# Performance work log

Hardware: AMD Instinct MI355X
Metric: run time of the kernel (lower is better)

## Reference

```python
import jax, jax.numpy as jnp
import numpy as np

# ---- constants hard-coded in the torch module ----
NEG_EPS = 1e-30          # eps used in log clamps
TAU = 0.35               # near-field temperature (getattr default)
K0 = 128                 # near-field band width
C_EMBD, N_HEADS, RANK = 768, 12, 32
B, T = 1, 2048


def _lin(k, fin, fout):
    lim = 1.0 / np.sqrt(fin)
    return jax.random.uniform(k, (fin, fout), jnp.float32, -lim, lim)


def _bias(k, fin, fout):
    lim = 1.0 / np.sqrt(fin)
    return jax.random.uniform(k, (fout,), jnp.float32, -lim, lim)


def setup_inputs() -> dict:
    key = jax.random.key(0)
    ks = jax.random.split(key, 24)
    C, H, R = C_EMBD, N_HEADS, RANK
    return {
        "x": jax.random.normal(ks[0], (B, T, C), jnp.float32),
        "Wq_w": _lin(ks[1], C, C), "Wq_b": _bias(ks[2], C, C),
        "Wk_w": _lin(ks[3], C, C), "Wk_b": _bias(ks[4], C, C),
        "Wv_w": _lin(ks[5], C, C), "Wv_b": _bias(ks[6], C, C),
        "Wo_w": _lin(ks[7], C, C), "Wo_b": _bias(ks[8], C, C),
        "Pq_w": _lin(ks[9], C, R),
        "Pk_w": _lin(ks[10], C, R),
        "Pv_w": _lin(ks[11], C, R),
        "up_w": _lin(ks[12], R, C),
        "gate_u": jax.random.normal(ks[13], (H, C // H), jnp.float32),
        "gate_b": jnp.zeros((H,), jnp.float32),
        "Wz_w": _lin(ks[14], 4 * C, C), "Wz_b": _bias(ks[15], 4 * C, C),
    }


def reference(x, Wq_w, Wq_b, Wk_w, Wk_b, Wv_w, Wv_b, Wo_w, Wo_b,
              Pq_w, Pk_w, Pv_w, up_w, gate_u, gate_b, Wz_w, Wz_b):
    Bx, Tx, C = x.shape
    H = gate_u.shape[0]
    D = C // H
    R = Pq_w.shape[1]
    k0 = min(K0, Tx - 1)
    kernel = k0 + 1
    b_scalar = -np.log(max(Tx, 1)).astype(np.float32) if hasattr(np.log(1.0), 'astype') else -np.log(max(Tx, 1))
    b_scalar = jnp.float32(-np.log(max(Tx, 1)))

    # 0) projections + heads
    Q = x @ Wq_w + Wq_b
    K = x @ Wk_w + Wk_b
    V = x @ Wv_w + Wv_b
    heads = lambda z: z.reshape(Bx, Tx, H, D).transpose(0, 2, 1, 3)  # (B,H,T,D)
    Qh, Kh, Vh = heads(Q), heads(K), heads(V)

    idx = jnp.arange(Tx)
    causal = idx[None, :] <= idx[:, None]                  # (T,T)
    band = causal & ((idx[:, None] - idx[None, :]) <= k0)  # banded causal

    # 1) low-rank EA + sigmoid + LASER seed
    Qr, Kr, Vr = Q @ Pq_w, K @ Pk_w, V @ Pv_w              # (B,T,R)
    S = (Qr @ Kr.transpose(0, 2, 1)) * (1.0 / np.sqrt(R))  # (B,T,T)
    # masked logits were -1e9 -> sigmoid == 0 exactly in fp32
    A_seed = jnp.where(causal[None], jax.nn.sigmoid(S * S + b_scalar), 0.0)
    # running causal max over keys, per feature (== amax of causally masked keys)
    m_seed = jax.lax.cummax(Vr, axis=1)                    # (B,T,R)
    Yr = jnp.einsum('bij,bjr->bir', A_seed, jnp.exp(Vr)) * jnp.exp(-m_seed)
    H0 = (jnp.log(jnp.maximum(Yr, NEG_EPS)) + m_seed) @ up_w  # (B,T,C)

    # 2a) near-field banded causal attention (cos^2 / tau, sigmoid, LASER)
    l2n = lambda z: z / jnp.maximum(jnp.linalg.norm(z, axis=-1, keepdims=True), 1e-12)
    cos = jnp.einsum('bhid,bhjd->bhij', l2n(Qh), l2n(Kh))  # (B,H,T,T)
    A_near = jnp.where(band[None, None], jax.nn.sigmoid(cos * cos / TAU + b_scalar), 0.0)
    # sliding-window (width kernel, past-only) max of V per feature
    m_near = jax.lax.reduce_window(
        Vh, -jnp.inf, jax.lax.max,
        window_dimensions=(1, 1, kernel, 1), window_strides=(1, 1, 1, 1),
        padding=[(0, 0), (0, 0), (kernel - 1, 0), (0, 0)])   # (B,H,T,D)
    V_exp = jnp.exp(Vh - m_near)
    Y_near = jnp.einsum('bhij,bhjd->bhid', A_near, V_exp)
    H_near = jnp.log(jnp.maximum(Y_near, NEG_EPS)) + m_near

    # 2b) far-field hierarchical levels: source truncates mid-loop; the
    # accumulator H_far_total_h is initialized to zeros -> contributes zero.
    Ht_h = H_near                                          # (B,H,T,D)

    # 3) head-wise sigmoid gating
    g = jax.nn.sigmoid(jnp.einsum('bhtd,hd->bht', Ht_h, gate_u) + gate_b[None, :, None])
    Ht_h = Ht_h * g[..., None]
    Htilde = Ht_h.transpose(0, 2, 1, 3).reshape(Bx, Tx, C)

    # 4) GRU blend (Wz consumes 4*C features)
    z = jax.nn.sigmoid(jnp.concatenate([x, H0, Htilde, H0 * Htilde], axis=-1) @ Wz_w + Wz_b)
    H_out = (1.0 - z) * H0 + z * Htilde
    return H_out @ Wo_w + Wo_b
```

## Files before the change

kernel.cpp:

```cpp
#include <hip/hip_runtime.h>
#include <math.h>

static constexpr float B_SCALAR    = -7.6246189861593985f;
static constexpr float INV_TAU     = 2.8571428571428571f;
static constexpr float INV_SQRT_R  = 0.17677669529663687f;

typedef __attribute__((ext_vector_type(8))) short bf16x8;
typedef __attribute__((ext_vector_type(4))) float f32x4;

__device__ __forceinline__ unsigned short f2b(float f) {
    union { float f; unsigned int u; } v; v.f = f;
    unsigned int r = v.u + 0x7fffu + ((v.u >> 16) & 1u);
    return (unsigned short)(r >> 16);
}

typedef const __attribute__((address_space(1))) unsigned int* gp1_t;
typedef __attribute__((address_space(3))) unsigned int* lp3_t;
__device__ __forceinline__ void gload16(const unsigned short* g, unsigned short* l) {
    __builtin_amdgcn_global_load_lds((gp1_t)g, (lp3_t)l, 16, 0, 0);
}

__device__ __forceinline__ bf16x8 frag128(const unsigned short* base, int row, int elem) {
    int byte = (row * 128 + elem * 2) ^ ((row & 7) << 4);
    return *(const bf16x8*)((const char*)base + byte);
}
__device__ __forceinline__ bf16x8 frag384(const unsigned short* base, int row, int elem) {
    int byte = (row * 384 + elem * 2) ^ ((row & 7) << 4);
    return *(const bf16x8*)((const char*)base + byte);
}

template<int MODE, int KZ>
__global__ __launch_bounds__(256) void gemm_mfma(
    const unsigned short* __restrict__ A0, const unsigned short* __restrict__ A1,
    const unsigned short* __restrict__ A2, const unsigned short* __restrict__ A3,
    const unsigned short* __restrict__ Bt, const float* __restrict__ bias,
    float* __restrict__ outf, unsigned short* __restrict__ outb,
    float* __restrict__ pbuf, int K, int ldo)
{
    __shared__ unsigned short As[2][128*64];
    __shared__ unsigned short Bs[2][128*64];
    const int tid = threadIdx.x;
    const int lane = tid & 63, wid = tid >> 6;
    const int wr = wid >> 1, wc = wid & 1;
    const int fr = lane & 15, fq = lane >> 4;
    const int n0 = blockIdx.x * 128, m0 = blockIdx.y * 128;
    const int kz = blockIdx.z;
    const int kslice = K / KZ;
    const int kbase = kz * kslice;
    const int nt = kslice / 64;

    f32x4 acc[4][4];
#pragma unroll
    for (int mi = 0; mi < 4; ++mi)
#pragma unroll
        for (int ni = 0; ni < 4; ++ni) acc[mi][ni] = (f32x4){0.f, 0.f, 0.f, 0.f};

    auto stage = [&](int buf, int k0) {
        const unsigned short* Ap;
        int k0l, ldA;
        if (MODE == 1) {
            int p = k0 / 768;
            Ap = (p == 0) ? A0 : (p == 1) ? A1 : (p == 2) ? A2 : A3;
            k0l = k0 - p * 768; ldA = 768;
        } else { Ap = A0; k0l = k0; ldA = K; }
#pragma unroll
        for (int i = 0; i < 4; ++i) {
            int cb = i * 256 + wid * 64;
            int c  = cb + lane;
            int r = c >> 3;
            int col = ((c & 7) ^ (r & 7)) * 8;
            gload16(Ap + (size_t)(m0 + r) * ldA + k0l + col, &As[buf][cb * 8]);
            gload16(Bt + (size_t)(n0 + r) * K   + k0  + col, &Bs[buf][cb * 8]);
        }
    };

    stage(0, kbase);
    asm volatile("s_waitcnt vmcnt(0)" ::: "memory");
    __builtin_amdgcn_s_barrier();
    __builtin_amdgcn_sched_barrier(0);

    int cur = 0;
    for (int t = 0; t < nt; ++t) {
        if (t + 1 < nt) stage(cur ^ 1, kbase + (t + 1) * 64);
#pragma unroll
        for (int kk = 0; kk < 64; kk += 32) {
            bf16x8 af[4], bfr[4];
#pragma unroll
            for (int mi = 0; mi < 4; ++mi)
                af[mi] = frag128(As[cur], wr*64 + mi*16 + fr, kk + fq*8);
#pragma unroll
            for (int ni = 0; ni < 4; ++ni)
                bfr[ni] = frag128(Bs[cur], wc*64 + ni*16 + fr, kk + fq*8);
#pragma unroll
            for (int mi = 0; mi < 4; ++mi)
#pragma unroll
                for (int ni = 0; ni < 4; ++ni)
                    acc[mi][ni] = __builtin_amdgcn_mfma_f32_16x16x32_bf16(
                        af[mi], bfr[ni], acc[mi][ni], 0, 0, 0);
        }
        asm volatile("s_waitcnt vmcnt(0)" ::: "memory");
        __builtin_amdgcn_s_barrier();
        __builtin_amdgcn_sched_barrier(0);
        cur ^= 1;
    }
#pragma unroll
    for (int mi = 0; mi < 4; ++mi)
#pragma unroll
        for (int ni = 0; ni < 4; ++ni)
#pragma unroll
            for (int v = 0; v < 4; ++v) {
                int m = m0 + wr*64 + mi*16 + fq*4 + v;
                int n = n0 + wc*64 + ni*16 + fr;
                float val = acc[mi][ni][v];
                if (KZ > 1) {
                    pbuf[((size_t)kz * 2048 + m) * 768 + n] = val;
                } else {
                    float vv = val + bias[n];
                    outf[(size_t)m * ldo + n] = vv;
                    if (MODE == 0) outb[(size_t)m * ldo + n] = f2b(vv);
                }
            }
}

__global__ __launch_bounds__(256) void wz_combine(
    const float* __restrict__ pbuf, const float* __restrict__ bz,
    const float* __restrict__ h0, const float* __restrict__ htl,
    unsigned short* __restrict__ outb)
{
    int i = blockIdx.x * 256 + threadIdx.x;
    if (i >= 2048*768/4) return;
    float4 s = *(const float4*)&pbuf[i*4];
    float4 p1 = *(const float4*)&pbuf[1536*1024 + i*4];
    float4 p2 = *(const float4*)&pbuf[2*1536*1024 + i*4];
    float4 p3 = *(const float4*)&pbuf[3*1536*1024 + i*4];
    s.x += p1.x + p2.x + p3.x; s.y += p1.y + p2.y + p3.y;
    s.z += p1.z + p2.z + p3.z; s.w += p1.w + p2.w + p3.w;
    float4 b = *(const float4*)&bz[(i % 192) * 4];
    float4 a = *(const float4*)&h0[i*4];
    float4 t = *(const float4*)&htl[i*4];
    float z0 = 1.f/(1.f+expf(-(s.x+b.x))), z1 = 1.f/(1.f+expf(-(s.y+b.y)));
    float z2 = 1.f/(1.f+expf(-(s.z+b.z))), z3 = 1.f/(1.f+expf(-(s.w+b.w)));
    outb[i*4+0] = f2b((1.f-z0)*a.x + z0*t.x);
    outb[i*4+1] = f2b((1.f-z1)*a.y + z1*t.y);
    outb[i*4+2] = f2b((1.f-z2)*a.z + z2*t.z);
    outb[i*4+3] = f2b((1.f-z3)*a.w + z3*t.w);
}

__global__ __launch_bounds__(256) void wo_combine(
    const float* __restrict__ pbuf, const float* __restrict__ bo,
    float* __restrict__ out)
{
    int i = blockIdx.x * 256 + threadIdx.x;
    if (i >= 2048*768/4) return;
    float4 s = *(const float4*)&pbuf[i*4];
    float4 p1 = *(const float4*)&pbuf[1536*1024 + i*4];
    float4 b = *(const float4*)&bo[(i % 192) * 4];
    float4 o;
    o.x = s.x + p1.x + b.x; o.y = s.y + p1.y + b.y;
    o.z = s.z + p1.z + b.z; o.w = s.w + p1.w + b.w;
    *(float4*)&out[i*4] = o;
}

__global__ __launch_bounds__(256) void prep_all(
    const float* __restrict__ x, unsigned short* __restrict__ xb,
    const float* __restrict__ wq, const float* __restrict__ wk,
    const float* __restrict__ wv, unsigned short* __restrict__ wqkvT,
    const float* __restrict__ wz, unsigned short* __restrict__ wzT,
    const float* __restrict__ wo, unsigned short* __restrict__ woT,
    const float* __restrict__ pq, const float* __restrict__ pk,
    const float* __restrict__ pv, unsigned short* __restrict__ pT,
    const float* __restrict__ bq, const float* __restrict__ bk,
    const float* __restrict__ bv, float* __restrict__ bqkv)
{
    __shared__ float tile[32][33];
    int b = blockIdx.x;
    if (b < 1536) {
        int i = b * 256 + threadIdx.x;
        float4 v = *(const float4*)&x[i * 4];
        xb[i*4+0] = f2b(v.x); xb[i*4+1] = f2b(v.y);
        xb[i*4+2] = f2b(v.z); xb[i*4+3] = f2b(v.w);
        return;
    }
    b -= 1536;
    const float* src; unsigned short* dst; int K, N, tb;
    if (b < 1728) {
        int sel = b / 576;
        src = (sel == 0) ? wq : (sel == 1) ? wk : wv;
        dst = wqkvT + (size_t)sel * 768 * 768;
        K = 768; N = 768; tb = b - sel * 576;
    } else if (b < 4032) {
        src = wz; dst = wzT; K = 3072; N = 768; tb = b - 1728;
    } else if (b < 4608) {
        src = wo; dst = woT; K = 768; N = 768; tb = b - 4032;
    } else if (b < 4680) {
        int sel = (b - 4608) / 24;
        src = (sel == 0) ? pq : (sel == 1) ? pk : pv;
        dst = pT + (size_t)sel * 32 * 768;
        K = 768; N = 32; tb = (b - 4608) % 24;
    } else {
        int n = (b - 4680) * 256 + threadIdx.x;
        if (n < 2304)
            bqkv[n] = (n < 768) ? bq[n] : (n < 1536) ? bk[n - 768] : bv[n - 1536];
        return;
    }
    int kt = K / 32;
    int kb = (tb % kt) * 32, nb = (tb / kt) * 32;
    int tx = threadIdx.x & 31, ty = threadIdx.x >> 5;
#pragma unroll
    for (int s = 0; s < 32; s += 8)
        tile[ty + s][tx] = src[(size_t)(kb + ty + s) * N + nb + tx];
    __syncthreads();
#pragma unroll
    for (int s = 0; s < 32; s += 8)
        dst[(size_t)(nb + ty + s) * K + kb + tx] = f2b(tile[tx][ty + s]);
}

__global__ __launch_bounds__(256) void lowrank_mfma(
    const unsigned short* __restrict__ qkvb, const unsigned short* __restrict__ pT,
    float* __restrict__ pbuf)
{
    __shared__ unsigned short As[2][128*64];
    __shared__ unsigned short Bs[2][32*64];
    const int tid = threadIdx.x, lane = tid & 63, wid = tid >> 6;
    const int fr = lane & 15, fq = lane >> 4;
    const int m0 = blockIdx.x * 128;
    const int sel = blockIdx.y, kz = blockIdx.z;
    const int kbase = kz * 192;

    f32x4 acc[2][2];
#pragma unroll
    for (int mi = 0; mi < 2; ++mi)
#pragma unroll
        for (int ni = 0; ni < 2; ++ni) acc[mi][ni] = (f32x4){0.f,0.f,0.f,0.f};

    auto stage = [&](int buf, int k0) {
#pragma unroll
        for (int i = 0; i < 4; ++i) {
            int cb = i * 256 + wid * 64, c = cb + lane;
            int r = c >> 3, col = ((c & 7) ^ (r & 7)) * 8;
            gload16(qkvb + (size_t)(m0 + r) * 2304 + sel*768 + k0 + col, &As[buf][cb * 8]);
        }
        {
            int cb = wid * 64, c = cb + lane;
            int r = c >> 3, col = ((c & 7) ^ (r & 7)) * 8;
            gload16(pT + (size_t)sel * 32*768 + (size_t)r * 768 + k0 + col, &Bs[buf][cb * 8]);
        }
    };

    stage(0, kbase);
    asm volatile("s_waitcnt vmcnt(0)" ::: "memory");
    __builtin_amdgcn_s_barrier();
    __builtin_amdgcn_sched_barrier(0);

    int cur = 0;
    for (int t = 0; t < 3; ++t) {
        if (t + 1 < 3) stage(cur ^ 1, kbase + (t + 1) * 64);
#pragma unroll
        for (int kk = 0; kk < 64; kk += 32) {
            bf16x8 a[2], b[2];
#pragma unroll
            for (int mi = 0; mi < 2; ++mi)
                a[mi] = frag128(As[cur], wid*32 + mi*16 + fr, kk + fq*8);
#pragma unroll
            for (int ni = 0; ni < 2; ++ni)
                b[ni] = frag128(Bs[cur], ni*16 + fr, kk + fq*8);
#pragma unroll
            for (int mi = 0; mi < 2; ++mi)
#pragma unroll
                for (int ni = 0; ni < 2; ++ni)
                    acc[mi][ni] = __builtin_amdgcn_mfma_f32_16x16x32_bf16(
                        a[mi], b[ni], acc[mi][ni], 0, 0, 0);
        }
        asm volatile("s_waitcnt vmcnt(0)" ::: "memory");
        __builtin_amdgcn_s_barrier();
        __builtin_amdgcn_sched_barrier(0);
        cur ^= 1;
    }
#pragma unroll
    for (int mi = 0; mi < 2; ++mi)
#pragma unroll
        for (int ni = 0; ni < 2; ++ni)
#pragma unroll
            for (int v = 0; v < 4; ++v) {
                int m = m0 + wid*32 + mi*16 + fq*4 + v;
                int n = ni*16 + fr;
                pbuf[((size_t)(kz*3 + sel) * 2048 + m) * 32 + n] = acc[mi][ni][v];
            }
}

__global__ __launch_bounds__(256) void lowrank_finish(
    const float* __restrict__ pbuf,
    unsigned short* __restrict__ qrb, unsigned short* __restrict__ krb,
    float* __restrict__ vr, unsigned short* __restrict__ evtb)
{
    int idx = blockIdx.x * 256 + threadIdx.x;
    int sel = idx >> 16, rem = idx & 65535;
    float s = pbuf[(size_t)(0*3 + sel)*65536 + rem]
            + pbuf[(size_t)(1*3 + sel)*65536 + rem]
            + pbuf[(size_t)(2*3 + sel)*65536 + rem]
            + pbuf[(size_t)(3*3 + sel)*65536 + rem];
    if (sel == 0)      qrb[rem] = f2b(s * INV_SQRT_R);
    else if (sel == 1) krb[rem] = f2b(s);
    else {
        int t = rem >> 5, r = rem & 31;
        vr[rem] = s;
        evtb[(size_t)r * 2048 + t] = f2b(expf(s));
    }
}

__global__ __launch_bounds__(256) void cummax_vr(const float* __restrict__ vr,
                                                 float* __restrict__ ms)
{
    __shared__ float part[256];
    int r = blockIdx.x, tid = threadIdx.x;
    int t0 = tid * 8;
    float v[8];
    float run = -INFINITY;
#pragma unroll
    for (int e = 0; e < 8; ++e) { run = fmaxf(run, vr[(t0+e)*32 + r]); v[e] = run; }
    part[tid] = run;
    __syncthreads();
    for (int off = 1; off < 256; off <<= 1) {
        float other = (tid >= off) ? part[tid - off] : -INFINITY;
        __syncthreads();
        part[tid] = fmaxf(part[tid], other);
        __syncthreads();
    }
    float excl = (tid > 0) ? part[tid - 1] : -INFINITY;
#pragma unroll
    for (int e = 0; e < 8; ++e) ms[(t0+e)*32 + r] = fmaxf(v[e], excl);
}

__global__ __launch_bounds__(256) void seed_mfma(
    const unsigned short* __restrict__ qrb, const unsigned short* __restrict__ krb,
    const unsigned short* __restrict__ evtb, float* __restrict__ partial)
{
    int it = blockIdx.x, jc = blockIdx.y;
    if (jc > it) return;
    const int i0 = it * 128, j0 = jc * 128;
    __shared__ unsigned short Qs[128*32];
    __shared__ unsigned short Ks[128*32];
    __shared__ unsigned short Es[32*128];
    __shared__ unsigned short Ps[128*128];
    const int tid = threadIdx.x, lane = tid & 63, wid = tid >> 6;
    const int fr = lane & 15, fq = lane >> 4;

#pragma unroll
    for (int s = 0; s < 2; ++s) {
        int cb = s * 256 + wid * 64;
        int c = cb + lane;
        int r = c >> 2, col = (c & 3) * 8;
        gload16(qrb + (size_t)(i0 + r) * 32 + col, &Qs[cb * 8]);
        gload16(krb + (size_t)(j0 + r) * 32 + col, &Ks[cb * 8]);
    }
#pragma unroll
    for (int s = 0; s < 2; ++s) {
        int c = s * 256 + tid;
        int rr = c >> 4, cc = c & 15;
        bf16x8 v = *(const bf16x8*)&evtb[(size_t)rr * 2048 + j0 + cc * 8];
        int byte = (rr * 256 + cc * 16) ^ ((rr & 7) << 4);
        *(bf16x8*)((char*)Es + byte) = v;
    }
    __syncthreads();

    const int wr = wid >> 1, wc = wid & 1;
    bf16x8 af[4], bk[4];
#pragma unroll
    for (int mi = 0; mi < 4; ++mi)
        af[mi] = *(const bf16x8*)&Qs[(wr*64 + mi*16 + fr)*32 + fq*8];
#pragma unroll
    for (int ni = 0; ni < 4; ++ni)
        bk[ni] = *(const bf16x8*)&Ks[(wc*64 + ni*16 + fr)*32 + fq*8];
#pragma unroll
    for (int mi = 0; mi < 4; ++mi)
#pragma unroll
        for (int ni = 0; ni < 4; ++ni) {
            f32x4 s4 = __builtin_amdgcn_mfma_f32_16x16x32_bf16(
                af[mi], bk[ni], (f32x4){0.f,0.f,0.f,0.f}, 0, 0, 0);
#pragma unroll
            for (int v = 0; v < 4; ++v) {
                int row = wr*64 + mi*16 + fq*4 + v;
                int col = wc*64 + ni*16 + fr;
                float a = 0.f;
                if (j0 + col <= i0 + row) {
                    float s = s4[v];
                    a = 1.f / (1.f + expf(-(s*s + B_SCALAR)));
                }
                int byte = (row * 256 + col * 2) ^ ((row & 7) << 4);
                *(unsigned short*)((char*)Ps + byte) = f2b(a);
            }
        }
    __syncthreads();

    f32x4 yacc[2][2];
#pragma unroll
    for (int mi = 0; mi < 2; ++mi)
#pragma unroll
        for (int nf = 0; nf < 2; ++nf) yacc[mi][nf] = (f32x4){0.f,0.f,0.f,0.f};
#pragma unroll
    for (int ks = 0; ks < 4; ++ks) {
        bf16x8 pa[2], eb[2];
#pragma unroll
        for (int mi = 0; mi < 2; ++mi) {
            int row = wid*32 + mi*16 + fr;
            int byte = (row * 256 + ks * 64 + fq * 16) ^ ((row & 7) << 4);
            pa[mi] = *(const bf16x8*)((const char*)Ps + byte);
        }
#pragma unroll
        for (int nf = 0; nf < 2; ++nf) {
            int rrow = nf*16 + fr;
            int byte = (rrow * 256 + ks * 64 + fq * 16) ^ ((rrow & 7) << 4);
            eb[nf] = *(const bf16x8*)((const char*)Es + byte);
        }
#pragma unroll
        for (int mi = 0; mi < 2; ++mi)
#pragma unroll
            for (int nf = 0; nf < 2; ++nf)
                yacc[mi][nf] = __builtin_amdgcn_mfma_f32_16x16x32_bf16(
                    pa[mi], eb[nf], yacc[mi][nf], 0, 0, 0);
    }
    float* pout = partial + ((size_t)(it*16 + jc) * 128) * 32;
#pragma unroll
    for (int mi = 0; mi < 2; ++mi)
#pragma unroll
        for (int nf = 0; nf < 2; ++nf)
#pragma unroll
            for (int v = 0; v < 4; ++v) {
                int row = wid*32 + mi*16 + fq*4 + v;
                int col = nf*16 + fr;
                pout[row*32 + col] = yacc[mi][nf][v];
            }
}

__global__ __launch_bounds__(256) void seed_up(
    const float* __restrict__ partial, const float* __restrict__ ms,
    const float* __restrict__ up, float* __restrict__ h0,
    unsigned short* __restrict__ h0b)
{
    __shared__ float ls[32];
    int t = blockIdx.x, tid = threadIdx.x;
    if (tid < 32) {
        int r = tid;
        int it = t >> 7, row = t & 127;
        float y = 0.f;
        for (int jjc = 0; jjc <= it; ++jjc)
            y += partial[(((size_t)(it*16 + jjc) * 128) + row) * 32 + r];
        float m = ms[t*32 + r];
        ls[r] = logf(fmaxf(y * expf(-m), 1e-30f)) + m;
    }
    __syncthreads();
    for (int c = tid; c < 768; c += 256) {
        float acc = 0.f;
#pragma unroll
        for (int rr = 0; rr < 32; ++rr) acc = fmaf(ls[rr], up[rr*768 + c], acc);
        h0[(size_t)t*768 + c] = acc;
        h0b[(size_t)t*768 + c] = f2b(acc);
    }
}

__global__ void head_norms_write(const float* __restrict__ qkv,
                                 unsigned short* __restrict__ qhatb,
                                 unsigned short* __restrict__ khatb)
{
    int t = blockIdx.x, tid = threadIdx.x;
    int h = tid >> 6, d = tid & 63;
    float q = qkv[t*2304 + h*64 + d];
    float k = qkv[t*2304 + 768 + h*64 + d];
    float sq = q*q, sk = k*k;
#pragma unroll
    for (int off = 32; off; off >>= 1) { sq += __shfl_xor(sq, off); sk += __shfl_xor(sk, off); }
    float iq = 1.f / fmaxf(sqrtf(sq), 1e-12f);
    float ik = 1.f / fmaxf(sqrtf(sk), 1e-12f);
    qhatb[(size_t)t*768 + h*64 + d] = f2b(q * iq);
    khatb[(size_t)t*768 + h*64 + d] = f2b(k * ik);
}

__global__ __launch_bounds__(256) void slide_max(const float* __restrict__ qkv,
                                                 float* __restrict__ mnear,
                                                 unsigned short* __restrict__ vexptb)
{
    __shared__ float vs[192][64];
    int c0 = blockIdx.x * 64, t0 = blockIdx.y * 64;
    int tid = threadIdx.x;
#pragma unroll
    for (int s = 0; s < 12; ++s) {
        int idx = tid + s * 256;
        int rr = idx >> 4, c4 = (idx & 15) * 4;
        int t = t0 - 128 + rr;
        float4 v4;
        if (t < 0) v4 = make_float4(-INFINITY, -INFINITY, -INFINITY, -INFINITY);
        else       v4 = *(const float4*)&qkv[t*2304 + 1536 + c0 + c4];
        *(float4*)&vs[rr][c4] = v4;
    }
    __syncthreads();
    int c = tid & 63, tg = tid >> 6;
    const int TG = tg * 16;
    float core = -INFINITY;
    for (int s = TG + 15; s <= TG + 128; ++s) core = fmaxf(core, vs[s][c]);
    float head[16], tail[16];
    head[15] = -INFINITY;
    float hs = -INFINITY;
#pragma unroll
    for (int u = 14; u >= 0; --u) { hs = fmaxf(hs, vs[TG + u][c]); head[u] = hs; }
    tail[0] = -INFINITY;
    float ts = -INFINITY;
#pragma unroll
    for (int u = 1; u <= 15; ++u) { ts = fmaxf(ts, vs[TG + 128 + u][c]); tail[u] = ts; }
#pragma unroll
    for (int u = 0; u < 16; ++u) {
        int tl = TG + u;
        float m = fmaxf(fmaxf(core, head[u]), tail[u]);
        float v = vs[tl + 128][c];
        int t = t0 + tl;
        mnear[(size_t)t*768 + c0 + c] = m;
        vexptb[(size_t)(c0 + c) * 2048 + t] = f2b(expf(v - m));
    }
}

__global__ __launch_bounds__(256) void near_fused(
    const unsigned short* __restrict__ qhatb, const unsigned short* __restrict__ khatb,
    const unsigned short* __restrict__ vexptb, const float* __restrict__ mnear,
    const float* __restrict__ gu, const float* __restrict__ gb,
    const float* __restrict__ h0, float* __restrict__ hn,
    unsigned short* __restrict__ htlb, unsigned short* __restrict__ prodb)
{
    __shared__ unsigned short Qs[64*64];
    __shared__ unsigned short KPs[192*64];
    __shared__ unsigned short Vst[64*192];
    const int it = blockIdx.x, hh = blockIdx.y;
    const int i0 = it * 64;
    const int tid = threadIdx.x, lane = tid & 63, wid = tid >> 6;
    const int fr = lane & 15, fq = lane >> 4;

#pragma unroll
    for (int i = 0; i < 2; ++i) {
        int cb = i * 256 + wid * 64, c = cb + lane;
        int r = c >> 3, col = ((c & 7) ^ (r & 7)) * 8;
        gload16(qhatb + (size_t)(i0 + r) * 768 + hh*64 + col, &Qs[cb * 8]);
    }
#pragma unroll
    for (int i = 0; i < 6; ++i) {
        int cb = i * 256 + wid * 64, c = cb + lane;
        int r = c >> 3, col = ((c & 7) ^ (r & 7)) * 8;
        int j = i0 - 128 + r; if (j < 0) j = 0;
        gload16(khatb + (size_t)j * 768 + hh*64 + col, &KPs[cb * 8]);
    }
#pragma unroll
    for (int i = 0; i < 6; ++i) {
        int cb = i * 256 + wid * 64, c = cb + lane;
        int d = c / 24, cc = c - d * 24;
        int ccp = (cc & 24) | ((cc & 7) ^ (d & 7));
        int t = i0 - 128 + ccp * 8; if (t < 0) t = 0;
        gload16(vexptb + (size_t)(hh*64 + d) * 2048 + t, &Vst[cb * 8]);
    }
    __syncthreads();

    f32x4 sacc[4][3];
#pragma unroll
    for (int mi = 0; mi < 4; ++mi)
#pragma unroll
        for (int ni = 0; ni < 3; ++ni) sacc[mi][ni] = (f32x4){0.f,0.f,0.f,0.f};
#pragma unroll
    for (int kt = 0; kt < 2; ++kt) {
        int kk = kt * 32;
        bf16x8 qa[4], kb[3];
#pragma unroll
        for (int mi = 0; mi < 4; ++mi)
            qa[mi] = frag128(Qs, mi*16 + fr, kk + fq*8);
#pragma unroll
        for (int ni = 0; ni < 3; ++ni)
            kb[ni] = frag128(KPs, wid*48 + ni*16 + fr, kk + fq*8);
#pragma unroll
        for (int mi = 0; mi < 4; ++mi)
#pragma unroll
            for (int ni = 0; ni < 3; ++ni)
                sacc[mi][ni] = __builtin_amdgcn_mfma_f32_16x16x32_bf16(
                    qa[mi], kb[ni], sacc[mi][ni], 0, 0, 0);
    }
    __syncthreads();

#pragma unroll
    for (int mi = 0; mi < 4; ++mi)
#pragma unroll
        for (int ni = 0; ni < 3; ++ni)
#pragma unroll
            for (int v = 0; v < 4; ++v) {
                int il = mi*16 + fq*4 + v;
                int jl = wid*48 + ni*16 + fr;
                float s = sacc[mi][ni][v];
                float a = 0.f;
                if (jl >= il && jl <= il + 128 && (i0 - 128 + jl) >= 0)
                    a = 1.f / (1.f + expf(-(s*s*INV_TAU + B_SCALAR)));
                int byte = (il * 384 + jl * 2) ^ ((il & 7) << 4);
                *(unsigned short*)((char*)KPs + byte) = f2b(a);
            }
    __syncthreads();

    f32x4 yacc[4];
#pragma unroll
    for (int nf = 0; nf < 4; ++nf) yacc[nf] = (f32x4){0.f,0.f,0.f,0.f};
#pragma unroll
    for (int ks = 0; ks < 6; ++ks) {
        int kk = ks * 32;
        bf16x8 pa = frag384(KPs, wid*16 + fr, kk + fq*8);
        bf16x8 vb[4];
#pragma unroll
        for (int nf = 0; nf < 4; ++nf)
            vb[nf] = frag384(Vst, nf*16 + fr, kk + fq*8);
#pragma unroll
        for (int nf = 0; nf < 4; ++nf)
            yacc[nf] = __builtin_amdgcn_mfma_f32_16x16x32_bf16(pa, vb[nf], yacc[nf], 0, 0, 0);
    }

    float hv[4][4];
    float sp[4] = {0.f, 0.f, 0.f, 0.f};
#pragma unroll
    for (int nf = 0; nf < 4; ++nf) {
        int d = nf*16 + fr;
        float guv = gu[hh*64 + d];
#pragma unroll
        for (int v = 0; v < 4; ++v) {
            int row = wid*16 + fq*4 + v;
            float y = yacc[nf][v];
            float h = logf(fmaxf(y, 1e-30f)) + mnear[(size_t)(i0 + row)*768 + hh*64 + d];
            hv[nf][v] = h;
            sp[v] = fmaf(h, guv, sp[v]);
        }
    }
#pragma unroll
    for (int off = 1; off < 16; off <<= 1) {
#pragma unroll
        for (int v = 0; v < 4; ++v) sp[v] += __shfl_xor(sp[v], off);
    }
    float gbh = gb[hh];
#pragma unroll
    for (int v = 0; v < 4; ++v) sp[v] = 1.f / (1.f + expf(-(sp[v] + gbh)));
#pragma unroll
    for (int nf = 0; nf < 4; ++nf)
#pragma unroll
        for (int v = 0; v < 4; ++v) {
            int row = wid*16 + fq*4 + v;
            int d = nf*16 + fr;
            size_t idx = (size_t)(i0 + row)*768 + hh*64 + d;
            float htl = hv[nf][v] * sp[v];
            hn[idx] = htl;
            htlb[idx] = f2b(htl);
            prodb[idx] = f2b(h0[idx] * htl);
        }
}

extern "C" void kernel_launch(void* const* d_in, const int* in_sizes, int n_in,
                              void* d_out, int out_size, void* d_ws, size_t ws_size,
                              hipStream_t stream)
{
    const float* x  = (const float*)d_in[0];
    const float* wq = (const float*)d_in[1];  const float* bq = (const float*)d_in[2];
    const float* wk = (const float*)d_in[3];  const float* bk = (const float*)d_in[4];
    const float* wv = (const float*)d_in[5];  const float* bv = (const float*)d_in[6];
    const float* wo = (const float*)d_in[7];  const float* bo = (const float*)d_in[8];
    const float* pq = (const float*)d_in[9];  const float* pk = (const float*)d_in[10];
    const float* pv = (const float*)d_in[11];
    const float* up = (const float*)d_in[12];
    const float* gu = (const float*)d_in[13]; const float* gb = (const float*)d_in[14];
    const float* wz = (const float*)d_in[15]; const float* bz = (const float*)d_in[16];
    float* out = (float*)d_out;

    float* w = (float*)d_ws;
    float* qkv  = w; w += 2048*2304;
    float* vr   = w; w += 2048*32;
    float* ms   = w; w += 2048*32;
    float* h0   = w; w += 2048*768;
    float* mnear= w; w += 2048*768;
    float* hn   = w; w += 2048*768;
    float* partial = w; w += 16*16*128*32;
    float* pgemm = w; w += 4*2048*768;
    float* plr   = w; w += 4*3*2048*32;
    float* bqkv = w; w += 2304;
    unsigned short* xb     = (unsigned short*)w; w += 2048*768/2;
    unsigned short* qkvb   = (unsigned short*)w; w += 2048*2304/2;
    unsigned short* wqkvT  = (unsigned short*)w; w += 2304*768/2;
    unsigned short* wzT    = (unsigned short*)w; w += 768*3072/2;
    unsigned short* woT    = (unsigned short*)w; w += 768*768/2;
    unsigned short* pT     = (unsigned short*)w; w += 3*32*768/2;
    unsigned short* h0b    = (unsigned short*)w; w += 2048*768/2;
    unsigned short* htlb   = (unsigned short*)w; w += 2048*768/2;
    unsigned short* prodb  = (unsigned short*)w; w += 2048*768/2;
    unsigned short* houtb  = (unsigned short*)w; w += 2048*768/2;
    unsigned short* qrb    = (unsigned short*)w; w += 2048*32/2;
    unsigned short* krb    = (unsigned short*)w; w += 2048*32/2;
    unsigned short* evtb   = (unsigned short*)w; w += 32*2048/2;
    unsigned short* qhatb  = (unsigned short*)w; w += 2048*768/2;
    unsigned short* khatb  = (unsigned short*)w; w += 2048*768/2;
    unsigned short* vexptb = (unsigned short*)w; w += 768*2048/2;

    prep_all<<<6225, 256, 0, stream>>>(x, xb, wq, wk, wv, wqkvT, wz, wzT,
                                       wo, woT, pq, pk, pv, pT, bq, bk, bv, bqkv);

    gemm_mfma<0,1><<<dim3(18,16,1), 256, 0, stream>>>(xb, nullptr, nullptr, nullptr,
        wqkvT, bqkv, qkv, qkvb, nullptr, 768, 2304);

    lowrank_mfma<<<dim3(16,3,4), 256, 0, stream>>>(qkvb, pT, plr);
    lowrank_finish<<<768, 256, 0, stream>>>(plr, qrb, krb, vr, evtb);
    cummax_vr<<<32, 256, 0, stream>>>(vr, ms);
    seed_mfma<<<dim3(16,16), 256, 0, stream>>>(qrb, krb, evtb, partial);
    seed_up<<<2048, 256, 0, stream>>>(partial, ms, up, h0, h0b);

    head_norms_write<<<2048, 768, 0, stream>>>(qkv, qhatb, khatb);
    slide_max<<<dim3(12,32), 256, 0, stream>>>(qkv, mnear, vexptb);
    near_fused<<<dim3(32,12), 256, 0, stream>>>(qhatb, khatb, vexptb, mnear,
                                                gu, gb, h0, hn, htlb, prodb);

    gemm_mfma<1,4><<<dim3(6,16,4), 256, 0, stream>>>(xb, h0b, htlb, prodb,
        wzT, nullptr, nullptr, nullptr, pgemm, 3072, 768);
    wz_combine<<<1536, 256, 0, stream>>>(pgemm, bz, h0, hn, houtb);
    gemm_mfma<2,2><<<dim3(6,16,2), 256, 0, stream>>>(houtb, nullptr, nullptr, nullptr,
        woT, nullptr, nullptr, nullptr, pgemm, 768, 768);
    wo_combine<<<1536, 256, 0, stream>>>(pgemm, bo, out);
}
```

Baseline: 148.2 us.

## Halve GEMM M-tile and merge small post-processing kernels into fewer launches

The shared GEMM kernel drops from 128x128 to 64x128 output tiles, doubling grid rows so more workgroups fill the device's compute units for these modest-sized matmuls. In exchange each block reuses its B tile over fewer rows. lowrank_finish and cummax_vr are merged into one kernel that reduces the Vr partials and runs the cumulative max directly, which removes the vr buffer and one launch. head_norms_write and slide_max are also fused into a single launch that picks its role from the block index.

```diff
diff --git a/kernel.cpp b/kernel.cpp
--- a/kernel.cpp
+++ b/kernel.cpp
@@ -37,21 +37,21 @@
     float* __restrict__ outf, unsigned short* __restrict__ outb,
     float* __restrict__ pbuf, int K, int ldo)
 {
-    __shared__ unsigned short As[2][128*64];
+    __shared__ unsigned short As[2][64*64];
     __shared__ unsigned short Bs[2][128*64];
     const int tid = threadIdx.x;
     const int lane = tid & 63, wid = tid >> 6;
     const int wr = wid >> 1, wc = wid & 1;
     const int fr = lane & 15, fq = lane >> 4;
-    const int n0 = blockIdx.x * 128, m0 = blockIdx.y * 128;
+    const int n0 = blockIdx.x * 128, m0 = blockIdx.y * 64;
     const int kz = blockIdx.z;
     const int kslice = K / KZ;
     const int kbase = kz * kslice;
     const int nt = kslice / 64;
 
-    f32x4 acc[4][4];
-#pragma unroll
-    for (int mi = 0; mi < 4; ++mi)
+    f32x4 acc[2][4];
+#pragma unroll
+    for (int mi = 0; mi < 2; ++mi)
 #pragma unroll
         for (int ni = 0; ni < 4; ++ni) acc[mi][ni] = (f32x4){0.f, 0.f, 0.f, 0.f};
 
@@ -64,13 +64,18 @@
             k0l = k0 - p * 768; ldA = 768;
         } else { Ap = A0; k0l = k0; ldA = K; }
 #pragma unroll
-        for (int i = 0; i < 4; ++i) {
-            int cb = i * 256 + wid * 64;
-            int c  = cb + lane;
+        for (int i = 0; i < 2; ++i) {
+            int cb = i * 256 + wid * 64, c = cb + lane;
             int r = c >> 3;
             int col = ((c & 7) ^ (r & 7)) * 8;
             gload16(Ap + (size_t)(m0 + r) * ldA + k0l + col, &As[buf][cb * 8]);
-            gload16(Bt + (size_t)(n0 + r) * K   + k0  + col, &Bs[buf][cb * 8]);
+        }
+#pragma unroll
+        for (int i = 0; i < 4; ++i) {
+            int cb = i * 256 + wid * 64, c = cb + lane;
+            int r = c >> 3;
+            int col = ((c & 7) ^ (r & 7)) * 8;
+            gload16(Bt + (size_t)(n0 + r) * K + k0 + col, &Bs[buf][cb * 8]);
         }
     };
 
@@ -84,15 +89,15 @@
         if (t + 1 < nt) stage(cur ^ 1, kbase + (t + 1) * 64);
 #pragma unroll
         for (int kk = 0; kk < 64; kk += 32) {
-            bf16x8 af[4], bfr[4];
-#pragma unroll
-            for (int mi = 0; mi < 4; ++mi)
-                af[mi] = frag128(As[cur], wr*64 + mi*16 + fr, kk + fq*8);
+            bf16x8 af[2], bfr[4];
+#pragma unroll
+            for (int mi = 0; mi < 2; ++mi)
+                af[mi] = frag128(As[cur], wr*32 + mi*16 + fr, kk + fq*8);
 #pragma unroll
             for (int ni = 0; ni < 4; ++ni)
                 bfr[ni] = frag128(Bs[cur], wc*64 + ni*16 + fr, kk + fq*8);
 #pragma unroll
-            for (int mi = 0; mi < 4; ++mi)
+            for (int mi = 0; mi < 2; ++mi)
 #pragma unroll
                 for (int ni = 0; ni < 4; ++ni)
                     acc[mi][ni] = __builtin_amdgcn_mfma_f32_16x16x32_bf16(
@@ -104,12 +109,12 @@
         cur ^= 1;
     }
 #pragma unroll
-    for (int mi = 0; mi < 4; ++mi)
+    for (int mi = 0; mi < 2; ++mi)
 #pragma unroll
         for (int ni = 0; ni < 4; ++ni)
 #pragma unroll
             for (int v = 0; v < 4; ++v) {
-                int m = m0 + wr*64 + mi*16 + fq*4 + v;
+                int m = m0 + wr*32 + mi*16 + fq*4 + v;
                 int n = n0 + wc*64 + ni*16 + fr;
                 float val = acc[mi][ni][v];
                 if (KZ > 1) {
@@ -288,36 +293,39 @@
             }
 }
 
-__global__ __launch_bounds__(256) void lowrank_finish(
+__global__ __launch_bounds__(256) void lowrank_post(
     const float* __restrict__ pbuf,
     unsigned short* __restrict__ qrb, unsigned short* __restrict__ krb,
-    float* __restrict__ vr, unsigned short* __restrict__ evtb)
-{
-    int idx = blockIdx.x * 256 + threadIdx.x;
-    int sel = idx >> 16, rem = idx & 65535;
-    float s = pbuf[(size_t)(0*3 + sel)*65536 + rem]
-            + pbuf[(size_t)(1*3 + sel)*65536 + rem]
-            + pbuf[(size_t)(2*3 + sel)*65536 + rem]
-            + pbuf[(size_t)(3*3 + sel)*65536 + rem];
-    if (sel == 0)      qrb[rem] = f2b(s * INV_SQRT_R);
-    else if (sel == 1) krb[rem] = f2b(s);
-    else {
-        int t = rem >> 5, r = rem & 31;
-        vr[rem] = s;
-        evtb[(size_t)r * 2048 + t] = f2b(expf(s));
-    }
-}
-
-__global__ __launch_bounds__(256) void cummax_vr(const float* __restrict__ vr,
-                                                 float* __restrict__ ms)
-{
+    unsigned short* __restrict__ evtb, float* __restrict__ ms)
+{
+    int b = blockIdx.x, tid = threadIdx.x;
+    if (b < 512) {
+        int idx = b * 256 + tid;
+        int sel = idx >> 16, rem = idx & 65535;
+        float s = pbuf[(size_t)(0*3 + sel)*65536 + rem]
+                + pbuf[(size_t)(1*3 + sel)*65536 + rem]
+                + pbuf[(size_t)(2*3 + sel)*65536 + rem]
+                + pbuf[(size_t)(3*3 + sel)*65536 + rem];
+        if (sel == 0) qrb[rem] = f2b(s * INV_SQRT_R);
+        else          krb[rem] = f2b(s);
+        return;
+    }
     __shared__ float part[256];
-    int r = blockIdx.x, tid = threadIdx.x;
+    int r = b - 512;
     int t0 = tid * 8;
-    float v[8];
+    float sv[8], v[8];
     float run = -INFINITY;
 #pragma unroll
-    for (int e = 0; e < 8; ++e) { run = fmaxf(run, vr[(t0+e)*32 + r]); v[e] = run; }
+    for (int e = 0; e < 8; ++e) {
+        int t = t0 + e;
+        float s = pbuf[(size_t)(0*3 + 2)*65536 + t*32 + r]
+                + pbuf[(size_t)(1*3 + 2)*65536 + t*32 + r]
+                + pbuf[(size_t)(2*3 + 2)*65536 + t*32 + r]
+                + pbuf[(size_t)(3*3 + 2)*65536 + t*32 + r];
+        sv[e] = s;
+        run = fmaxf(run, s);
+        v[e] = run;
+    }
     part[tid] = run;
     __syncthreads();
     for (int off = 1; off < 256; off <<= 1) {
@@ -328,7 +336,11 @@
     }
     float excl = (tid > 0) ? part[tid - 1] : -INFINITY;
 #pragma unroll
-    for (int e = 0; e < 8; ++e) ms[(t0+e)*32 + r] = fmaxf(v[e], excl);
+    for (int e = 0; e < 8; ++e) {
+        int t = t0 + e;
+        ms[t*32 + r] = fmaxf(v[e], excl);
+        evtb[(size_t)r * 2048 + t] = f2b(expf(sv[e]));
+    }
 }
 
 __global__ __launch_bounds__(256) void seed_mfma(
@@ -458,30 +470,30 @@
     }
 }
 
-__global__ void head_norms_write(const float* __restrict__ qkv,
-                                 unsigned short* __restrict__ qhatb,
-                                 unsigned short* __restrict__ khatb)
-{
-    int t = blockIdx.x, tid = threadIdx.x;
-    int h = tid >> 6, d = tid & 63;
-    float q = qkv[t*2304 + h*64 + d];
-    float k = qkv[t*2304 + 768 + h*64 + d];
-    float sq = q*q, sk = k*k;
-#pragma unroll
-    for (int off = 32; off; off >>= 1) { sq += __shfl_xor(sq, off); sk += __shfl_xor(sk, off); }
-    float iq = 1.f / fmaxf(sqrtf(sq), 1e-12f);
-    float ik = 1.f / fmaxf(sqrtf(sk), 1e-12f);
-    qhatb[(size_t)t*768 + h*64 + d] = f2b(q * iq);
-    khatb[(size_t)t*768 + h*64 + d] = f2b(k * ik);
-}
-
-__global__ __launch_bounds__(256) void slide_max(const float* __restrict__ qkv,
-                                                 float* __restrict__ mnear,
-                                                 unsigned short* __restrict__ vexptb)
+__global__ __launch_bounds__(256) void norms_slide(
+    const float* __restrict__ qkv,
+    unsigned short* __restrict__ qhatb, unsigned short* __restrict__ khatb,
+    float* __restrict__ mnear, unsigned short* __restrict__ vexptb)
 {
     __shared__ float vs[192][64];
-    int c0 = blockIdx.x * 64, t0 = blockIdx.y * 64;
-    int tid = threadIdx.x;
+    int b = blockIdx.x, tid = threadIdx.x;
+    if (b < 6144) {
+        int w = b * 4 + (tid >> 6);
+        int lane = tid & 63;
+        int t = w / 12, h = w - t * 12;
+        float q = qkv[t*2304 + h*64 + lane];
+        float k = qkv[t*2304 + 768 + h*64 + lane];
+        float sq = q*q, sk = k*k;
+#pragma unroll
+        for (int off = 32; off; off >>= 1) { sq += __shfl_xor(sq, off); sk += __shfl_xor(sk, off); }
+        float iq = 1.f / fmaxf(sqrtf(sq), 1e-12f);
+        float ik = 1.f / fmaxf(sqrtf(sk), 1e-12f);
+        qhatb[(size_t)t*768 + h*64 + lane] = f2b(q * iq);
+        khatb[(size_t)t*768 + h*64 + lane] = f2b(k * ik);
+        return;
+    }
+    b -= 6144;
+    int c0 = (b % 12) * 64, t0 = (b / 12) * 64;
 #pragma unroll
     for (int s = 0; s < 12; ++s) {
         int idx = tid + s * 256;
@@ -667,7 +679,6 @@
 
     float* w = (float*)d_ws;
     float* qkv  = w; w += 2048*2304;
-    float* vr   = w; w += 2048*32;
     float* ms   = w; w += 2048*32;
     float* h0   = w; w += 2048*768;
     float* mnear= w; w += 2048*768;
@@ -696,24 +707,22 @@
     prep_all<<<6225, 256, 0, stream>>>(x, xb, wq, wk, wv, wqkvT, wz, wzT,
                                        wo, woT, pq, pk, pv, pT, bq, bk, bv, bqkv);
 
-    gemm_mfma<0,1><<<dim3(18,16,1), 256, 0, stream>>>(xb, nullptr, nullptr, nullptr,
+    gemm_mfma<0,1><<<dim3(18,32,1), 256, 0, stream>>>(xb, nullptr, nullptr, nullptr,
         wqkvT, bqkv, qkv, qkvb, nullptr, 768, 2304);
 
     lowrank_mfma<<<dim3(16,3,4), 256, 0, stream>>>(qkvb, pT, plr);
-    lowrank_finish<<<768, 256, 0, stream>>>(plr, qrb, krb, vr, evtb);
-    cummax_vr<<<32, 256, 0, stream>>>(vr, ms);
+    lowrank_post<<<544, 256, 0, stream>>>(plr, qrb, krb, evtb, ms);
     seed_mfma<<<dim3(16,16), 256, 0, stream>>>(qrb, krb, evtb, partial);
     seed_up<<<2048, 256, 0, stream>>>(partial, ms, up, h0, h0b);
 
-    head_norms_write<<<2048, 768, 0, stream>>>(qkv, qhatb, khatb);
-    slide_max<<<dim3(12,32), 256, 0, stream>>>(qkv, mnear, vexptb);
+    norms_slide<<<6528, 256, 0, stream>>>(qkv, qhatb, khatb, mnear, vexptb);
     near_fused<<<dim3(32,12), 256, 0, stream>>>(qhatb, khatb, vexptb, mnear,
                                                 gu, gb, h0, hn, htlb, prodb);
 
-    gemm_mfma<1,4><<<dim3(6,16,4), 256, 0, stream>>>(xb, h0b, htlb, prodb,
+    gemm_mfma<1,4><<<dim3(6,32,4), 256, 0, stream>>>(xb, h0b, htlb, prodb,
         wzT, nullptr, nullptr, nullptr, pgemm, 3072, 768);
     wz_combine<<<1536, 256, 0, stream>>>(pgemm, bz, h0, hn, houtb);
-    gemm_mfma<2,2><<<dim3(6,16,2), 256, 0, stream>>>(houtb, nullptr, nullptr, nullptr,
+    gemm_mfma<2,2><<<dim3(6,32,2), 256, 0, stream>>>(houtb, nullptr, nullptr, nullptr,
         woT, nullptr, nullptr, nullptr, pgemm, 768, 768);
     wo_combine<<<1536, 256, 0, stream>>>(pgemm, bo, out);
 }
```

Result: no change. 149.3 us (+0.7%).
